# Optimization experiments

Measured on AMD Instinct MI355X. Metric: run time of the kernel, lower is better.

Reference implementation:

```python
import jax, jax.numpy as jnp
import numpy as np

IN_DIM = 128
OUT_DIM = 128
B, N = 8, 2048
NEG_SLOPE = 0.2


def setup_inputs() -> dict:
    key = jax.random.key(0)
    k_h, k_adj, k_W, k_a = jax.random.split(key, 4)
    h = jax.random.normal(k_h, (B, N, IN_DIM), dtype=jnp.float32)
    adj = jax.random.randint(k_adj, (B, N, N), 0, 2, dtype=jnp.int32)
    # nn.Linear(in, out, bias=False): weight [out, in]
    W = jax.random.normal(k_W, (OUT_DIM, IN_DIM), dtype=jnp.float32) * (1.0 / np.sqrt(IN_DIM))
    # nn.Linear(2*out, 1, bias=False): weight [1, 2*out] -> store as vector [2*out]
    a = jax.random.normal(k_a, (2 * OUT_DIM,), dtype=jnp.float32) * (1.0 / np.sqrt(2 * OUT_DIM))
    return {"h": h, "adj": adj, "W": W, "a": a}


def reference(h, adj, W, a):
    # Wh: [B, N, Fo]
    Wh = jnp.einsum("bnf,of->bno", h, W)
    Fo = Wh.shape[-1]
    a_src, a_dst = a[:Fo], a[Fo:]
    # attn(cat([Wh_i, Wh_j])) == (Wh_i . a_src) + (Wh_j . a_dst) -- avoids [B,N,N,2F]
    s = Wh @ a_src  # [B, N]
    t = Wh @ a_dst  # [B, N]
    e = jax.nn.leaky_relu(s[:, :, None] + t[:, None, :], negative_slope=NEG_SLOPE)  # [B,N,N]
    e = jnp.where(adj == 0, -jnp.inf, e)
    alpha = jax.nn.softmax(e, axis=-1)
    alpha = jnp.nan_to_num(alpha, nan=0.0)  # rows with no neighbors -> 0
    return jnp.einsum("bnm,bmo->bno", alpha, Wh)
```

## Files before the change

### kernel.cpp

```cpp
#include <hip/hip_runtime.h>
#include <hip/hip_bf16.h>
#include <hip/hip_fp16.h>
#include <math.h>

#define B_ 8
#define N_ 2048
#define F_ 128

typedef __attribute__((ext_vector_type(8))) _Float16 half8;
typedef __attribute__((ext_vector_type(4))) float f32x4;

__global__ __launch_bounds__(256) void k_wh(
    const float* __restrict__ h, const float* __restrict__ W,
    const float* __restrict__ a,
    _Float16* __restrict__ WhH, float* __restrict__ sv, float* __restrict__ tv)
{
    __shared__ float h_s[64][129];
    __shared__ float Wt[128][68];
    __shared__ float wsm[128], wtm[128];
    __shared__ float sred[64][4], tred[64][4];

    const int t = threadIdx.x;
    const int rowblk = blockIdx.x >> 1;
    const int ohalf  = blockIdx.x & 1;
    const int r0 = rowblk * 64;

    {
        const int f = (t & 31) * 4;
        #pragma unroll
        for (int it = 0; it < 8; ++it) {
            const int r = (t >> 5) + it * 8;
            float4 v = *(const float4*)&h[(size_t)(r0 + r) * F_ + f];
            h_s[r][f] = v.x; h_s[r][f + 1] = v.y;
            h_s[r][f + 2] = v.z; h_s[r][f + 3] = v.w;
        }
    }
    {
        const int f = (t & 31) * 4;
        #pragma unroll
        for (int it = 0; it < 8; ++it) {
            const int o = (t >> 5) + it * 8;
            float4 v = *(const float4*)&W[(size_t)(ohalf * 64 + o) * F_ + f];
            Wt[f][o] = v.x; Wt[f + 1][o] = v.y;
            Wt[f + 2][o] = v.z; Wt[f + 3][o] = v.w;
        }
    }
    {
        const int f = t & 127;
        const int which = t >> 7;
        const float* av = a + which * 128;
        float acc = 0.f;
        for (int o = 0; o < 128; ++o)
            acc += W[(size_t)o * F_ + f] * av[o];
        if (which == 0) wsm[f] = acc; else wtm[f] = acc;
    }
    __syncthreads();

    const int o4 = t & 15;
    const int r4 = t >> 4;
    float acc[4][4];
    #pragma unroll
    for (int i = 0; i < 4; ++i)
        #pragma unroll
        for (int j = 0; j < 4; ++j) acc[i][j] = 0.f;

    #pragma unroll 4
    for (int k = 0; k < 128; ++k) {
        float4 w = *(const float4*)&Wt[k][o4 * 4];
        float h0 = h_s[r4 * 4 + 0][k];
        float h1 = h_s[r4 * 4 + 1][k];
        float h2 = h_s[r4 * 4 + 2][k];
        float h3 = h_s[r4 * 4 + 3][k];
        acc[0][0] += h0 * w.x; acc[0][1] += h0 * w.y; acc[0][2] += h0 * w.z; acc[0][3] += h0 * w.w;
        acc[1][0] += h1 * w.x; acc[1][1] += h1 * w.y; acc[1][2] += h1 * w.z; acc[1][3] += h1 * w.w;
        acc[2][0] += h2 * w.x; acc[2][1] += h2 * w.y; acc[2][2] += h2 * w.z; acc[2][3] += h2 * w.w;
        acc[3][0] += h3 * w.x; acc[3][1] += h3 * w.y; acc[3][2] += h3 * w.z; acc[3][3] += h3 * w.w;
    }

    {
        const int Rbase = r0 + r4 * 4;
        const int b    = Rbase >> 11;
        const int jj   = Rbase & 2047;
        const int jblk = jj >> 5;
        const int k8   = (jj >> 3) & 3;
        const int kk   = jj & 7;
        #pragma unroll
        for (int jo = 0; jo < 4; ++jo) {
            const int o = ohalf * 64 + o4 * 4 + jo;
            size_t off = ((size_t)(b * 64 + jblk) * 128 + o) * 32 + k8 * 8 + kk;
            union { _Float16 x[4]; uint2 u; } pk;
            pk.x[0] = (_Float16)acc[0][jo];
            pk.x[1] = (_Float16)acc[1][jo];
            pk.x[2] = (_Float16)acc[2][jo];
            pk.x[3] = (_Float16)acc[3][jo];
            *(uint2*)(WhH + off) = pk.u;
        }
    }

    {
        const int r = t & 63, part = t >> 6;
        float as_ = 0.f, at_ = 0.f;
        const int kb = part * 32;
        for (int k = kb; k < kb + 32; ++k) {
            float hv = h_s[r][k];
            as_ += hv * wsm[k];
            at_ += hv * wtm[k];
        }
        sred[r][part] = as_; tred[r][part] = at_;
    }
    __syncthreads();
    if (ohalf == 0 && t < 64) {
        sv[r0 + t] = sred[t][0] + sred[t][1] + sred[t][2] + sred[t][3];
        tv[r0 + t] = tred[t][0] + tred[t][1] + tred[t][2] + tred[t][3];
    }
}

__global__ __launch_bounds__(256) void k_attn(
    const _Float16* __restrict__ WhH, const float* __restrict__ sv,
    const float* __restrict__ tv, const int* __restrict__ adj,
    float* __restrict__ out)
{
    __shared__ _Float16 Pl[2][16][40];
    __shared__ float il[16];
    __shared__ float tmr[4];

    const int t  = threadIdx.x;
    const int b  = blockIdx.x >> 7;
    const int i0 = (blockIdx.x & 127) * 16;
    const float* tb = tv + ((size_t)b << 11);

    float tm = -INFINITY;
    #pragma unroll
    for (int k = 0; k < 8; ++k) tm = fmaxf(tm, tb[t + k * 256]);
    #pragma unroll
    for (int k = 32; k; k >>= 1) tm = fmaxf(tm, __shfl_xor(tm, k, 64));
    if ((t & 63) == 0) tmr[t >> 6] = tm;
    __syncthreads();
    const float tmax = fmaxf(fmaxf(tmr[0], tmr[1]), fmaxf(tmr[2], tmr[3]));

    const int i_a = t >> 5;
    const int jl  = t & 31;
    const float s0 = sv[((size_t)b << 11) + i0 + i_a];
    const float s1 = sv[((size_t)b << 11) + i0 + i_a + 8];
    const float M0 = fmaxf(s0 + tmax, 0.f);
    const float M1 = fmaxf(s1 + tmax, 0.f);

    const int* arow0 = adj + ((size_t)(((size_t)b << 11) + i0 + i_a) << 11);
    const int* arow1 = arow0 + ((size_t)8 << 11);

    const int lane = t & 63;
    const int wv   = t >> 6;
    const int m_   = lane & 15;
    const int q_   = lane >> 4;

    f32x4 accA = {0.f, 0.f, 0.f, 0.f};
    f32x4 accB = {0.f, 0.f, 0.f, 0.f};
    float lsum0 = 0.f, lsum1 = 0.f;

    int   a0 = arow0[jl], a1 = arow1[jl];
    float tj = tb[jl];

    for (int jc = 0; jc < 64; ++jc) {
        const int jn = ((jc + 1) & 63) * 32;
        const int   na0 = arow0[jn + jl];
        const int   na1 = arow1[jn + jl];
        const float ntj = tb[jn + jl];

        const _Float16* wb = WhH + ((size_t)(b * 64 + jc) << 12) + q_ * 8;
        half8 bf0 = *(const half8*)(wb + (size_t)(wv * 32 + m_) * 32);
        half8 bf1 = *(const half8*)(wb + (size_t)(wv * 32 + 16 + m_) * 32);

        float e0 = s0 + tj; e0 = fmaxf(e0, 0.2f * e0);
        float p0 = a0 ? __expf(e0 - M0) : 0.f;
        float e1 = s1 + tj; e1 = fmaxf(e1, 0.2f * e1);
        float p1 = a1 ? __expf(e1 - M1) : 0.f;
        lsum0 += p0; lsum1 += p1;

        const int bufc = jc & 1;
        Pl[bufc][i_a][jl]     = (_Float16)p0;
        Pl[bufc][i_a + 8][jl] = (_Float16)p1;
        __syncthreads();

        half8 af = *(const half8*)&Pl[bufc][m_][q_ * 8];
        accA = __builtin_amdgcn_mfma_f32_16x16x32_f16(af, bf0, accA, 0, 0, 0);
        accB = __builtin_amdgcn_mfma_f32_16x16x32_f16(af, bf1, accB, 0, 0, 0);

        a0 = na0; a1 = na1; tj = ntj;
    }

    #pragma unroll
    for (int k = 16; k; k >>= 1) {
        lsum0 += __shfl_xor(lsum0, k, 64);
        lsum1 += __shfl_xor(lsum1, k, 64);
    }
    if (jl == 0) {
        il[i_a]     = lsum0 > 0.f ? 1.f / lsum0 : 0.f;
        il[i_a + 8] = lsum1 > 0.f ? 1.f / lsum1 : 0.f;
    }
    __syncthreads();

    float* outb = out + (((size_t)((b << 11) + i0)) << 7);
    #pragma unroll
    for (int reg = 0; reg < 4; ++reg) {
        const int row = q_ * 4 + reg;
        const float sc = il[row];
        outb[(size_t)row * 128 + wv * 32 + m_]      = accA[reg] * sc;
        outb[(size_t)row * 128 + wv * 32 + 16 + m_] = accB[reg] * sc;
    }
}

extern "C" void kernel_launch(void* const* d_in, const int* in_sizes, int n_in,
                              void* d_out, int out_size, void* d_ws, size_t ws_size,
                              hipStream_t stream) {
    const float* h   = (const float*)d_in[0];
    const int*   adj = (const int*)d_in[1];
    const float* W   = (const float*)d_in[2];
    const float* a   = (const float*)d_in[3];
    float* out = (float*)d_out;

    _Float16* WhH = (_Float16*)d_ws;
    float* sv = (float*)((char*)d_ws + (size_t)4 * 1024 * 1024);
    float* tv = sv + (size_t)B_ * N_;

    k_wh<<<512, 256, 0, stream>>>(h, W, a, WhH, sv, tv);
    k_attn<<<1024, 256, 0, stream>>>(WhH, sv, tv, adj, out);
}
```

Before: 241.0 us.

## Split key dimension across waves in attention kernel, reduce partials in LDS

Each wave now processes a quarter of the neighbor columns for all 16 rows and all 128 output features. Probabilities are computed directly in MFMA A-operand registers, so the per-chunk LDS staging and block-wide __syncthreads are gone. The four partial accumulators and row sums are reduced through shared memory at the end. This trades the loop barrier for more accumulator registers and a 32KB LDS reduction buffer, and adds a launch-bounds occupancy hint.

```diff
diff --git a/kernel.cpp b/kernel.cpp
--- a/kernel.cpp
+++ b/kernel.cpp
@@ -115,13 +115,13 @@
     }
 }
 
-__global__ __launch_bounds__(256) void k_attn(
+__global__ __launch_bounds__(256, 4) void k_attn(
     const _Float16* __restrict__ WhH, const float* __restrict__ sv,
     const float* __restrict__ tv, const int* __restrict__ adj,
     float* __restrict__ out)
 {
-    __shared__ _Float16 Pl[2][16][40];
-    __shared__ float il[16];
+    __shared__ float redO[4][16][128];
+    __shared__ float redL[4][16];
     __shared__ float tmr[4];
 
     const int t  = threadIdx.x;
@@ -138,74 +138,85 @@
     __syncthreads();
     const float tmax = fmaxf(fmaxf(tmr[0], tmr[1]), fmaxf(tmr[2], tmr[3]));
 
-    const int i_a = t >> 5;
-    const int jl  = t & 31;
-    const float s0 = sv[((size_t)b << 11) + i0 + i_a];
-    const float s1 = sv[((size_t)b << 11) + i0 + i_a + 8];
-    const float M0 = fmaxf(s0 + tmax, 0.f);
-    const float M1 = fmaxf(s1 + tmax, 0.f);
-
-    const int* arow0 = adj + ((size_t)(((size_t)b << 11) + i0 + i_a) << 11);
-    const int* arow1 = arow0 + ((size_t)8 << 11);
-
+    const int wv   = t >> 6;
     const int lane = t & 63;
-    const int wv   = t >> 6;
     const int m_   = lane & 15;
     const int q_   = lane >> 4;
 
-    f32x4 accA = {0.f, 0.f, 0.f, 0.f};
-    f32x4 accB = {0.f, 0.f, 0.f, 0.f};
-    float lsum0 = 0.f, lsum1 = 0.f;
-
-    int   a0 = arow0[jl], a1 = arow1[jl];
-    float tj = tb[jl];
-
-    for (int jc = 0; jc < 64; ++jc) {
-        const int jn = ((jc + 1) & 63) * 32;
-        const int   na0 = arow0[jn + jl];
-        const int   na1 = arow1[jn + jl];
-        const float ntj = tb[jn + jl];
-
-        const _Float16* wb = WhH + ((size_t)(b * 64 + jc) << 12) + q_ * 8;
-        half8 bf0 = *(const half8*)(wb + (size_t)(wv * 32 + m_) * 32);
-        half8 bf1 = *(const half8*)(wb + (size_t)(wv * 32 + 16 + m_) * 32);
-
-        float e0 = s0 + tj; e0 = fmaxf(e0, 0.2f * e0);
-        float p0 = a0 ? __expf(e0 - M0) : 0.f;
-        float e1 = s1 + tj; e1 = fmaxf(e1, 0.2f * e1);
-        float p1 = a1 ? __expf(e1 - M1) : 0.f;
-        lsum0 += p0; lsum1 += p1;
-
-        const int bufc = jc & 1;
-        Pl[bufc][i_a][jl]     = (_Float16)p0;
-        Pl[bufc][i_a + 8][jl] = (_Float16)p1;
-        __syncthreads();
-
-        half8 af = *(const half8*)&Pl[bufc][m_][q_ * 8];
-        accA = __builtin_amdgcn_mfma_f32_16x16x32_f16(af, bf0, accA, 0, 0, 0);
-        accB = __builtin_amdgcn_mfma_f32_16x16x32_f16(af, bf1, accB, 0, 0, 0);
-
-        a0 = na0; a1 = na1; tj = ntj;
-    }
-
-    #pragma unroll
-    for (int k = 16; k; k >>= 1) {
-        lsum0 += __shfl_xor(lsum0, k, 64);
-        lsum1 += __shfl_xor(lsum1, k, 64);
-    }
-    if (jl == 0) {
-        il[i_a]     = lsum0 > 0.f ? 1.f / lsum0 : 0.f;
-        il[i_a + 8] = lsum1 > 0.f ? 1.f / lsum1 : 0.f;
-    }
-    __syncthreads();
-
-    float* outb = out + (((size_t)((b << 11) + i0)) << 7);
-    #pragma unroll
-    for (int reg = 0; reg < 4; ++reg) {
-        const int row = q_ * 4 + reg;
-        const float sc = il[row];
-        outb[(size_t)row * 128 + wv * 32 + m_]      = accA[reg] * sc;
-        outb[(size_t)row * 128 + wv * 32 + 16 + m_] = accB[reg] * sc;
+    const float s_i = sv[((size_t)b << 11) + i0 + m_];
+    const float M_i = fmaxf(s_i + tmax, 0.f);
+
+    const int jbase = wv * 512;
+    const int* arow = adj + ((size_t)(((b << 11) + i0 + m_)) << 11) + q_ * 8;
+    const float* tq = tb + q_ * 8;
+    const _Float16* wbase = WhH + (((size_t)b * 64) << 12)
+                          + (size_t)m_ * 32 + q_ * 8;
+
+    f32x4 acc[8];
+    #pragma unroll
+    for (int n = 0; n < 8; ++n) acc[n] = (f32x4){0.f, 0.f, 0.f, 0.f};
+    float lsum = 0.f;
+
+    int4 aL = *(const int4*)&arow[jbase];
+    int4 aH = *(const int4*)&arow[jbase + 4];
+
+    for (int jj = 0; jj < 16; ++jj) {
+        const int j0 = jbase + jj * 32;
+        const int jn = jbase + ((jj + 1) & 15) * 32;
+        int4 naL = *(const int4*)&arow[jn];
+        int4 naH = *(const int4*)&arow[jn + 4];
+
+        float4 tL = *(const float4*)&tq[j0];
+        float4 tH = *(const float4*)&tq[j0 + 4];
+
+        float e, p[8];
+        e = s_i + tL.x; e = fmaxf(e, 0.2f * e); p[0] = aL.x ? __expf(e - M_i) : 0.f;
+        e = s_i + tL.y; e = fmaxf(e, 0.2f * e); p[1] = aL.y ? __expf(e - M_i) : 0.f;
+        e = s_i + tL.z; e = fmaxf(e, 0.2f * e); p[2] = aL.z ? __expf(e - M_i) : 0.f;
+        e = s_i + tL.w; e = fmaxf(e, 0.2f * e); p[3] = aL.w ? __expf(e - M_i) : 0.f;
+        e = s_i + tH.x; e = fmaxf(e, 0.2f * e); p[4] = aH.x ? __expf(e - M_i) : 0.f;
+        e = s_i + tH.y; e = fmaxf(e, 0.2f * e); p[5] = aH.y ? __expf(e - M_i) : 0.f;
+        e = s_i + tH.z; e = fmaxf(e, 0.2f * e); p[6] = aH.z ? __expf(e - M_i) : 0.f;
+        e = s_i + tH.w; e = fmaxf(e, 0.2f * e); p[7] = aH.w ? __expf(e - M_i) : 0.f;
+
+        lsum += ((p[0] + p[1]) + (p[2] + p[3])) + ((p[4] + p[5]) + (p[6] + p[7]));
+
+        half8 af;
+        #pragma unroll
+        for (int k = 0; k < 8; ++k) af[k] = (_Float16)p[k];
+
+        const _Float16* wb = wbase + ((size_t)(j0 >> 5) << 12);
+        #pragma unroll
+        for (int n = 0; n < 8; ++n) {
+            half8 bf = *(const half8*)(wb + n * 512);
+            acc[n] = __builtin_amdgcn_mfma_f32_16x16x32_f16(af, bf, acc[n], 0, 0, 0);
+        }
+        aL = naL; aH = naH;
+    }
+
+    lsum += __shfl_xor(lsum, 16, 64);
+    lsum += __shfl_xor(lsum, 32, 64);
+    if (q_ == 0) redL[wv][m_] = lsum;
+
+    #pragma unroll
+    for (int n = 0; n < 8; ++n)
+        #pragma unroll
+        for (int r = 0; r < 4; ++r)
+            redO[wv][q_ * 4 + r][n * 16 + m_] = acc[n][r];
+    __syncthreads();
+
+    {
+        const int row = t >> 4;
+        const int c0  = (t & 15) * 8;
+        const float li = redL[0][row] + redL[1][row] + redL[2][row] + redL[3][row];
+        const float sc = li > 0.f ? 1.f / li : 0.f;
+        float* op = out + (((size_t)((b << 11) + i0 + row)) << 7) + c0;
+        #pragma unroll
+        for (int c = 0; c < 8; ++c) {
+            float v = redO[0][row][c0 + c] + redO[1][row][c0 + c]
+                    + redO[2][row][c0 + c] + redO[3][row][c0 + c];
+            op[c] = v * sc;
+        }
     }
 }
 
```

Result: no change. 242.4 us (+0.6%).
